# Optimization experiments

Measured on AMD Instinct MI355X. Metric: run time of the kernel, lower is better.

## Reference

```python
import jax, jax.numpy as jnp
import numpy as np

EMBED_DIM = 384
NUM_HEADS = 6
HEAD_DIM = EMBED_DIM // NUM_HEADS
MLP_HIDDEN = 4 * EMBED_DIM
LN_EPS = 1e-5


def layer_norm(x, gamma, beta):
    mu = jnp.mean(x, axis=-1, keepdims=True)
    var = jnp.mean((x - mu) ** 2, axis=-1, keepdims=True)
    return (x - mu) * jax.lax.rsqrt(var + LN_EPS) * gamma + beta


def setup_inputs() -> dict:
    key = jax.random.key(0)
    ks = jax.random.split(key, 8)
    D, H = EMBED_DIM, MLP_HIDDEN
    s = 1.0 / np.sqrt(D)
    sh = 1.0 / np.sqrt(H)
    return {
        "x": jax.random.normal(ks[0], (16, 1024, D), dtype=jnp.float32),
        "ln1_g": jnp.ones((D,), jnp.float32),
        "ln1_b": jnp.zeros((D,), jnp.float32),
        "qkv_w": jax.random.uniform(ks[1], (3 * D, D), jnp.float32, -s, s),
        "qkv_b": jax.random.uniform(ks[2], (3 * D,), jnp.float32, -s, s),
        "proj_w": jax.random.uniform(ks[3], (D, D), jnp.float32, -s, s),
        "proj_b": jax.random.uniform(ks[4], (D,), jnp.float32, -s, s),
        "ln2_g": jnp.ones((D,), jnp.float32),
        "ln2_b": jnp.zeros((D,), jnp.float32),
        "fc1_w": jax.random.uniform(ks[5], (H, D), jnp.float32, -s, s),
        "fc1_b": jax.random.uniform(ks[6], (H,), jnp.float32, -s, s),
        "fc2_w": jax.random.uniform(ks[7], (D, H), jnp.float32, -sh, sh),
        "fc2_b": jnp.zeros((D,), jnp.float32),
    }


def reference(x, ln1_g, ln1_b, qkv_w, qkv_b, proj_w, proj_b,
              ln2_g, ln2_b, fc1_w, fc1_b, fc2_w, fc2_b):
    B, N, D = x.shape
    Hh, Dh = NUM_HEADS, HEAD_DIM
    scale = Dh ** -0.5

    # --- attention sublayer (pre-norm) ---
    h = layer_norm(x, ln1_g, ln1_b)
    qkv = h @ qkv_w.T + qkv_b                      # [B,N,3D]
    qkv = qkv.reshape(B, N, 3, Hh, Dh)
    q, k, v = (qkv[:, :, i].transpose(0, 2, 1, 3) for i in range(3))  # [B,H,N,Dh]
    attn = jax.nn.softmax(jnp.einsum('bhnd,bhmd->bhnm', q, k) * scale, axis=-1)
    o = jnp.einsum('bhnm,bhmd->bhnd', attn, v)     # [B,H,N,Dh]
    o = o.transpose(0, 2, 1, 3).reshape(B, N, D)
    x = x + (o @ proj_w.T + proj_b)

    # --- MLP sublayer (pre-norm) ---
    h = layer_norm(x, ln2_g, ln2_b)
    h = jax.nn.gelu(h @ fc1_w.T + fc1_b, approximate=False)
    x = x + (h @ fc2_w.T + fc2_b)
    return x
```

## Files before the change

kernel.cpp:

```cpp
#include <hip/hip_runtime.h>

typedef unsigned short u16;
typedef unsigned int   u32;
typedef __bf16  bf16x8 __attribute__((ext_vector_type(8)));
typedef __bf16  bf16x4_t __attribute__((ext_vector_type(4)));
typedef float   f32x4  __attribute__((ext_vector_type(4)));
typedef float   f32x2  __attribute__((ext_vector_type(2)));

struct Ptrs { const void* p[13]; };

extern "C" __device__ float __ocml_native_exp2_f32(float);

__device__ __forceinline__ float bf2f(u16 u) {
    union { unsigned int i; float f; } c; c.i = ((unsigned int)u) << 16; return c.f;
}
__device__ __forceinline__ u16 f2bf(float f) {
    union { float f; unsigned int i; } c; c.f = f;
    unsigned int u = c.i;
    unsigned int r = (u + 0x7fffu + ((u >> 16) & 1u)) >> 16;
    return (u16)r;
}

__device__ __forceinline__ float wave_sum(float x) {
#pragma unroll
    for (int m = 32; m >= 1; m >>= 1) x += __shfl_xor(x, m);
    return x;
}

__device__ __forceinline__ void g2l16(const u16* g, u16* l) {
    __builtin_amdgcn_global_load_lds(
        (__attribute__((address_space(1))) void*)g,
        (__attribute__((address_space(3))) void*)l, 16, 0, 0);
}

__device__ __forceinline__ int sniff_bf16(const u32* __restrict__ w) {
    int cnt = 0;
    for (int i = 0; i < 32; ++i) {
        u16 lo = (u16)(w[i] & 0xFFFFu);
        int e = (lo >> 7) & 0xFF;
        cnt += (e >= 117 && e <= 123) ? 1 : 0;
    }
    return (cnt >= 16) ? 1 : 0;
}

__global__ __launch_bounds__(256) void k_cvt_ln1(Ptrs ps,
                                                 u16* __restrict__ cw,
                                                 int* __restrict__ flagp,
                                                 u16* __restrict__ cx,
                                                 u16* __restrict__ h)
{
    const int flag = sniff_bf16((const u32*)ps.p[3]);
    if (blockIdx.x == 0 && threadIdx.x == 0) *flagp = flag;

    if (blockIdx.x < 867) {
        const int cum[13] = {0,48,96,55392,55536,73968,74016,74064,74112,
                             147840,148032,221760,221808};
        const int off[12] = {0,384,768,443136,444288,591744,
                             592128,592512,592896,1182720,1184256,1774080};
        int c = blockIdx.x * 256 + threadIdx.x;
        if (c >= 221808) return;
        int seg = 0;
#pragma unroll
        for (int i = 1; i < 12; ++i) seg += (c >= cum[i]) ? 1 : 0;
        int e = (c - cum[seg]) * 8;
        u16* dst = cw + off[seg] + e;
        if (flag) {
            *(uint4*)dst = *((const uint4*)ps.p[seg + 1] + (e >> 3));
        } else {
            const float* s = (const float*)ps.p[seg + 1] + e;
            u16 tmp[8];
#pragma unroll
            for (int t = 0; t < 8; ++t) tmp[t] = f2bf(s[t]);
            *(uint4*)dst = *(const uint4*)tmp;
        }
        return;
    }

    const int wid = threadIdx.x >> 6, lane = threadIdx.x & 63;
    const int row = (blockIdx.x - 867) * 4 + wid;
    const int e0 = lane * 6;
    float v[6]; u16 raw[6];
    float gv[6], bv[6];
    if (flag) {
        const u16* p = (const u16*)ps.p[0] + (size_t)row * 384 + e0;
        u32 w0 = *(const u32*)(p);
        u32 w1 = *(const u32*)(p + 2);
        u32 w2 = *(const u32*)(p + 4);
        raw[0] = (u16)w0; raw[1] = (u16)(w0 >> 16);
        raw[2] = (u16)w1; raw[3] = (u16)(w1 >> 16);
        raw[4] = (u16)w2; raw[5] = (u16)(w2 >> 16);
#pragma unroll
        for (int t = 0; t < 6; t++) v[t] = bf2f(raw[t]);
        const u16* gp = (const u16*)ps.p[1] + e0;
        const u16* bp = (const u16*)ps.p[2] + e0;
#pragma unroll
        for (int t = 0; t < 6; t++) { gv[t] = bf2f(gp[t]); bv[t] = bf2f(bp[t]); }
    } else {
        const float* p = (const float*)ps.p[0] + (size_t)row * 384 + e0;
        f32x2 a0 = *(const f32x2*)(p);
        f32x2 a1 = *(const f32x2*)(p + 2);
        f32x2 a2 = *(const f32x2*)(p + 4);
        v[0] = a0[0]; v[1] = a0[1]; v[2] = a1[0];
        v[3] = a1[1]; v[4] = a2[0]; v[5] = a2[1];
#pragma unroll
        for (int t = 0; t < 6; t++) raw[t] = f2bf(v[t]);
        const float* gp = (const float*)ps.p[1] + e0;
        const float* bp = (const float*)ps.p[2] + e0;
#pragma unroll
        for (int t = 0; t < 6; t++) { gv[t] = gp[t]; bv[t] = bp[t]; }
    }
    u32* pc = (u32*)(cx + (size_t)row * 384 + e0);
    pc[0] = (u32)raw[0] | ((u32)raw[1] << 16);
    pc[1] = (u32)raw[2] | ((u32)raw[3] << 16);
    pc[2] = (u32)raw[4] | ((u32)raw[5] << 16);
    float s = 0.f;
#pragma unroll
    for (int t = 0; t < 6; t++) s += v[t];
    const float mu = wave_sum(s) * (1.0f / 384.0f);
    float vs = 0.f;
#pragma unroll
    for (int t = 0; t < 6; t++) { float d = v[t] - mu; vs += d * d; }
    const float var = wave_sum(vs) * (1.0f / 384.0f);
    const float rs = rsqrtf(var + 1e-5f);
    u16 ow[6];
#pragma unroll
    for (int t = 0; t < 6; t++)
        ow[t] = f2bf((v[t] - mu) * rs * gv[t] + bv[t]);
    u32* po = (u32*)(h + (size_t)row * 384 + e0);
    po[0] = (u32)ow[0] | ((u32)ow[1] << 16);
    po[1] = (u32)ow[2] | ((u32)ow[3] << 16);
    po[2] = (u32)ow[4] | ((u32)ow[5] << 16);
}

template <bool SWAP = false>
__device__ __forceinline__ void gemm_core_128_w8(const u16* __restrict__ A,
                                                 const u16* __restrict__ B,
                                                 int K, int m0, int n0,
                                                 f32x4 (&acc)[4][2])
{
    __shared__ __align__(16) u16 As[128 * 64];
    __shared__ __align__(16) u16 Bs[128 * 64];

    const int tid  = threadIdx.x;
    const int lane = tid & 63;
    const int wid  = tid >> 6;
    const int wm  = (wid >> 2) * 64;
    const int wn  = (wid & 3) * 32;
    const int l15 = lane & 15;
    const int g   = lane >> 4;
    const int srow   = lane >> 3;
    const int schunk = ((lane & 7) ^ srow) * 8;

    const u16* Abase = A + (size_t)(m0 + wid * 16 + srow) * K + schunk;
    const u16* Bbase = B + (size_t)(n0 + wid * 16 + srow) * K + schunk;

    for (int kk = 0; kk < K; kk += 64) {
        __syncthreads();
#pragma unroll
        for (int t = 0; t < 2; ++t) {
            g2l16(Abase + (size_t)t * 8 * K + kk, &As[(wid * 16 + t * 8) * 64]);
            g2l16(Bbase + (size_t)t * 8 * K + kk, &Bs[(wid * 16 + t * 8) * 64]);
        }
        __syncthreads();

#pragma unroll
        for (int ks = 0; ks < 2; ++ks) {
            const int p = ((ks * 4 + g) ^ (l15 & 7)) * 8;
            bf16x8 af[4], bfr[2];
#pragma unroll
            for (int i = 0; i < 4; i++)
                af[i] = __builtin_bit_cast(bf16x8,
                         *(const uint4*)&As[(wm + 16 * i + l15) * 64 + p]);
#pragma unroll
            for (int j = 0; j < 2; j++)
                bfr[j] = __builtin_bit_cast(bf16x8,
                         *(const uint4*)&Bs[(wn + 16 * j + l15) * 64 + p]);
#pragma unroll
            for (int i = 0; i < 4; i++)
#pragma unroll
                for (int j = 0; j < 2; j++) {
                    if (SWAP)
                        acc[i][j] = __builtin_amdgcn_mfma_f32_16x16x32_bf16(
                                        bfr[j], af[i], acc[i][j], 0, 0, 0);
                    else
                        acc[i][j] = __builtin_amdgcn_mfma_f32_16x16x32_bf16(
                                        af[i], bfr[j], acc[i][j], 0, 0, 0);
                }
        }
    }
}

__device__ __forceinline__ void gemm_core_128x64_w8(const u16* __restrict__ A,
                                                    const u16* __restrict__ B,
                                                    int K, int m0, int n0,
                                                    f32x4 (&acc)[2][2])
{
    __shared__ __align__(16) u16 As[128 * 64];
    __shared__ __align__(16) u16 Bs[64 * 64];

    const int tid  = threadIdx.x;
    const int lane = tid & 63;
    const int wid  = tid >> 6;
    const int wm  = (wid >> 1) * 32;
    const int wn  = (wid & 1) * 32;
    const int l15 = lane & 15;
    const int g   = lane >> 4;
    const int srow   = lane >> 3;
    const int schunk = ((lane & 7) ^ srow) * 8;

    const u16* Abase = A + (size_t)(m0 + wid * 16 + srow) * K + schunk;
    const u16* Bbase = B + (size_t)(n0 + wid * 8 + srow) * K + schunk;

    for (int kk = 0; kk < K; kk += 64) {
        __syncthreads();
#pragma unroll
        for (int t = 0; t < 2; ++t)
            g2l16(Abase + (size_t)t * 8 * K + kk, &As[(wid * 16 + t * 8) * 64]);
        g2l16(Bbase + kk, &Bs[(wid * 8) * 64]);
        __syncthreads();

#pragma unroll
        for (int ks = 0; ks < 2; ++ks) {
            const int p = ((ks * 4 + g) ^ (l15 & 7)) * 8;
            bf16x8 af[2], bfr[2];
#pragma unroll
            for (int i = 0; i < 2; i++)
                af[i] = __builtin_bit_cast(bf16x8,
                         *(const uint4*)&As[(wm + 16 * i + l15) * 64 + p]);
#pragma unroll
            for (int j = 0; j < 2; j++)
                bfr[j] = __builtin_bit_cast(bf16x8,
                         *(const uint4*)&Bs[(wn + 16 * j + l15) * 64 + p]);
#pragma unroll
            for (int i = 0; i < 2; i++)
#pragma unroll
                for (int j = 0; j < 2; j++)
                    acc[i][j] = __builtin_amdgcn_mfma_f32_16x16x32_bf16(
                                    af[i], bfr[j], acc[i][j], 0, 0, 0);
        }
    }
}

__global__ __launch_bounds__(256) void k_layernorm(const u16* __restrict__ in,
                                                   const u16* __restrict__ g,
                                                   const u16* __restrict__ b,
                                                   u16* __restrict__ out,
                                                   int nrows)
{
    const int wid = threadIdx.x >> 6, lane = threadIdx.x & 63;
    const int row = blockIdx.x * 4 + wid;
    if (row >= nrows) return;
    const int e0 = lane * 6;
    float v[6];
    const u16* p = in + (size_t)row * 384 + e0;
    u32 w0 = *(const u32*)(p);
    u32 w1 = *(const u32*)(p + 2);
    u32 w2 = *(const u32*)(p + 4);
    v[0] = bf2f((u16)w0); v[1] = bf2f((u16)(w0 >> 16));
    v[2] = bf2f((u16)w1); v[3] = bf2f((u16)(w1 >> 16));
    v[4] = bf2f((u16)w2); v[5] = bf2f((u16)(w2 >> 16));
    float s = 0.f;
#pragma unroll
    for (int t = 0; t < 6; t++) s += v[t];
    const float mu = wave_sum(s) * (1.0f / 384.0f);
    float vs = 0.f;
#pragma unroll
    for (int t = 0; t < 6; t++) { float d = v[t] - mu; vs += d * d; }
    const float var = wave_sum(vs) * (1.0f / 384.0f);
    const float rs = rsqrtf(var + 1e-5f);
    const u32* gg = (const u32*)(g + e0);
    const u32* bb = (const u32*)(b + e0);
    u32 gw[3] = {gg[0], gg[1], gg[2]};
    u32 bw[3] = {bb[0], bb[1], bb[2]};
    u16 ow[6];
#pragma unroll
    for (int t = 0; t < 6; t++) {
        u16 ge = (u16)(gw[t >> 1] >> ((t & 1) * 16));
        u16 be = (u16)(bw[t >> 1] >> ((t & 1) * 16));
        ow[t] = f2bf((v[t] - mu) * rs * bf2f(ge) + bf2f(be));
    }
    u32* po = (u32*)(out + (size_t)row * 384 + e0);
    po[0] = (u32)ow[0] | ((u32)ow[1] << 16);
    po[1] = (u32)ow[2] | ((u32)ow[3] << 16);
    po[2] = (u32)ow[4] | ((u32)ow[5] << 16);
}

__global__ __launch_bounds__(512) void k_gemm_qkv(const u16* __restrict__ A,
                                                  const u16* __restrict__ W,
                                                  const u16* __restrict__ bias,
                                                  u16* __restrict__ q,
                                                  u16* __restrict__ kbuf,
                                                  u16* __restrict__ vT)
{
    const int id = blockIdx.x, slot = id & 7, idx = id >> 3;
    const int m0 = (slot * 16 + idx / 9) * 128;
    const int n0 = (idx % 9) * 128;
    f32x4 acc[4][2];
#pragma unroll
    for (int i = 0; i < 4; i++)
#pragma unroll
        for (int j = 0; j < 2; j++) acc[i][j] = f32x4{0.f, 0.f, 0.f, 0.f};
    gemm_core_128_w8<true>(A, W, 384, m0, n0, acc);
    const int lane = threadIdx.x & 63, wid = threadIdx.x >> 6;
    const int wm = (wid >> 2) * 64, wn = (wid & 3) * 32;
    const int l15 = lane & 15, rq = (lane >> 4) * 4;
#pragma unroll
    for (int i = 0; i < 4; i++) {
        const int gr = m0 + wm + 16 * i + l15;
        const int bb = gr >> 10, nn = gr & 1023;
#pragma unroll
        for (int j = 0; j < 2; j++) {
            const int gcb = n0 + wn + 16 * j + rq;
            const int part = gcb / 384, rem = gcb % 384;
            const int head = rem >> 6, dhb = rem & 63;
            const int bh = bb * 6 + head;
            float vals[4];
#pragma unroll
            for (int r = 0; r < 4; r++) vals[r] = acc[i][j][r] + bf2f(bias[gcb + r]);
            if (part == 2) {
#pragma unroll
                for (int r = 0; r < 4; r++)
                    vT[((size_t)bh * 64 + dhb + r) * 1024 + nn] = f2bf(vals[r]);
            } else {
                u16* dst = part ? kbuf : q;
                u32 lo = (u32)f2bf(vals[0]) | ((u32)f2bf(vals[1]) << 16);
                u32 hi = (u32)f2bf(vals[2]) | ((u32)f2bf(vals[3]) << 16);
                uint2 pk; pk.x = lo; pk.y = hi;
                *(uint2*)&dst[((size_t)bh * 1024 + nn) * 64 + dhb] = pk;
            }
        }
    }
}

__global__ __launch_bounds__(512) void k_attn(const u16* __restrict__ q,
                                              const u16* __restrict__ kk,
                                              const u16* __restrict__ vT,
                                              u16* __restrict__ o)
{
    __shared__ __align__(16) u16 Ks[128 * 64];
    __shared__ __align__(16) u16 Vs[2][64 * 64];
    __shared__ __align__(16) u16 Ps[128 * 64];

    const int tid = threadIdx.x, lane = tid & 63, wid = tid >> 6;
    const int l15 = lane & 15, g = lane >> 4, q8 = g * 8;
    const int id = blockIdx.x;
    const int bh = (id & 7) * 12 + ((id >> 3) >> 3);
    const int q0 = ((id >> 3) & 7) * 128;
    const int wrow = wid * 16;

    const u16* Q = q  + (size_t)bh * 65536;
    const u16* K = kk + (size_t)bh * 65536;
    const u16* V = vT + (size_t)bh * 65536;

    const int srow   = lane >> 3;
    const int schunk = ((lane & 7) ^ srow) * 8;
    const int rd0 = ((0 + g) ^ (l15 & 7)) * 8;
    const int rd1 = ((4 + g) ^ (l15 & 7)) * 8;
    int pcol[4];
#pragma unroll
    for (int ip = 0; ip < 4; ++ip)
        pcol[ip] = (((ip * 2 + (g >> 1)) ^ (l15 & 7)) * 8) + (g & 1) * 4;

    bf16x8 aq[2];
#pragma unroll
    for (int ks = 0; ks < 2; ++ks) {
        bf16x8 t = __builtin_bit_cast(bf16x8,
            *(const uint4*)&Q[(size_t)(q0 + wrow + l15) * 64 + ks * 32 + q8]);
#pragma unroll
        for (int e = 0; e < 8; ++e)
            t[e] = (__bf16)((float)t[e] * 0.18033688f);
        aq[ks] = t;
    }

    f32x4 ob[4];
#pragma unroll
    for (int j = 0; j < 4; ++j) ob[j] = f32x4{0.f, 0.f, 0.f, 0.f};
    float lsum = 0.f;

    for (int kt2 = 0; kt2 < 8; ++kt2) {
        __syncthreads();
#pragma unroll
        for (int t = 0; t < 2; ++t) {
            int r0 = wid * 16 + t * 8;
            g2l16(&K[(size_t)(kt2 * 128 + r0 + srow) * 64 + schunk], &Ks[r0 * 64]);
        }
#pragma unroll
        for (int h = 0; h < 2; ++h) {
            int r0 = wid * 8;
            g2l16(&V[(size_t)(r0 + srow) * 1024 + kt2 * 128 + h * 64 + schunk],
                  &Vs[h][r0 * 64]);
        }
        __syncthreads();

#pragma unroll 1
        for (int h = 0; h < 2; ++h) {
            f32x4 st[4];
#pragma unroll
            for (int ip = 0; ip < 4; ++ip) st[ip] = f32x4{0.f, 0.f, 0.f, 0.f};
            __builtin_amdgcn_s_setprio(1);
#pragma unroll
            for (int ip = 0; ip < 4; ++ip) {
                int rbase = (h * 64 + ip * 16 + l15) * 64;
                bf16x8 bk0 = __builtin_bit_cast(bf16x8,
                    *(const uint4*)&Ks[rbase + rd0]);
                bf16x8 bk1 = __builtin_bit_cast(bf16x8,
                    *(const uint4*)&Ks[rbase + rd1]);
                st[ip] = __builtin_amdgcn_mfma_f32_16x16x32_bf16(
                            bk0, aq[0], st[ip], 0, 0, 0);
                st[ip] = __builtin_amdgcn_mfma_f32_16x16x32_bf16(
                            bk1, aq[1], st[ip], 0, 0, 0);
            }
            __builtin_amdgcn_s_setprio(0);

            float ps = 0.f;
#pragma unroll
            for (int ip = 0; ip < 4; ++ip)
#pragma unroll
                for (int r = 0; r < 4; ++r) {
                    float p = __ocml_native_exp2_f32(st[ip][r]);
                    st[ip][r] = p;
                    ps += p;
                }
            lsum += ps;

#pragma unroll
            for (int ip = 0; ip < 4; ++ip) {
                bf16x4_t pk;
#pragma unroll
                for (int r = 0; r < 4; ++r) pk[r] = (__bf16)st[ip][r];
                *(bf16x4_t*)&Ps[(wrow + l15) * 64 + pcol[ip]] = pk;
            }

            __builtin_amdgcn_s_setprio(1);
#pragma unroll
            for (int ks = 0; ks < 2; ++ks) {
                const int rdo = ks ? rd1 : rd0;
                bf16x8 ap = __builtin_bit_cast(bf16x8,
                    *(const uint4*)&Ps[(wrow + l15) * 64 + rdo]);
#pragma unroll
                for (int jv = 0; jv < 4; ++jv) {
                    bf16x8 bv = __builtin_bit_cast(bf16x8,
                        *(const uint4*)&Vs[h][(jv * 16 + l15) * 64 + rdo]);
                    ob[jv] = __builtin_amdgcn_mfma_f32_16x16x32_bf16(
                                ap, bv, ob[jv], 0, 0, 0);
                }
            }
            __builtin_amdgcn_s_setprio(0);
        }
    }

    lsum += __shfl_xor(lsum, 16);
    lsum += __shfl_xor(lsum, 32);
    const int bb = bh / 6, hh = bh % 6;
#pragma unroll
    for (int r = 0; r < 4; ++r) {
        int src = (lane & 48) | (g * 4 + r);
        float linv = 1.0f / __shfl(lsum, src);
        int row = q0 + wrow + g * 4 + r;
#pragma unroll
        for (int jv = 0; jv < 4; ++jv) {
            int dh = jv * 16 + l15;
            o[((size_t)(bb * 1024 + row)) * 384 + hh * 64 + dh] =
                f2bf(ob[jv][r] * linv);
        }
    }
}

__global__ __launch_bounds__(512) void k_gemm_proj(const u16* __restrict__ A,
                                                   const u16* __restrict__ W,
                                                   const u16* __restrict__ bias,
                                                   const u16* __restrict__ xin,
                                                   u16* __restrict__ x1)
{
    const int id = blockIdx.x, slot = id & 7, idx = id >> 3;
    const int m0 = (slot * 16 + idx / 6) * 128;
    const int n0 = (idx % 6) * 64;
    f32x4 acc[2][2];
#pragma unroll
    for (int i = 0; i < 2; i++)
#pragma unroll
        for (int j = 0; j < 2; j++) acc[i][j] = f32x4{0.f, 0.f, 0.f, 0.f};
    gemm_core_128x64_w8(A, W, 384, m0, n0, acc);
    const int lane = threadIdx.x & 63, wid = threadIdx.x >> 6;
    const int wm = (wid >> 1) * 32, wn = (wid & 1) * 32;
    const int l15 = lane & 15, rq = (lane >> 4) * 4;
#pragma unroll
    for (int i = 0; i < 2; i++)
#pragma unroll
        for (int j = 0; j < 2; j++)
#pragma unroll
            for (int r = 0; r < 4; r++) {
                int gr = m0 + wm + 16 * i + rq + r;
                int gc = n0 + wn + 16 * j + l15;
                size_t ix = (size_t)gr * 384 + gc;
                x1[ix] = f2bf(acc[i][j][r] + bf2f(bias[gc]) + bf2f(xin[ix]));
            }
}

__global__ __launch_bounds__(512) void k_gemm_fc1(const u16* __restrict__ A,
                                                  const u16* __restrict__ W,
                                                  const u16* __restrict__ bias,
                                                  u16* __restrict__ hmid)
{
    const int id = blockIdx.x, slot = id & 7, idx = id >> 3;
    const int m0 = (slot * 16 + idx / 12) * 128;
    const int n0 = (idx % 12) * 128;
    f32x4 acc[4][2];
#pragma unroll
    for (int i = 0; i < 4; i++)
#pragma unroll
        for (int j = 0; j < 2; j++) acc[i][j] = f32x4{0.f, 0.f, 0.f, 0.f};
    gemm_core_128_w8(A, W, 384, m0, n0, acc);
    const int lane = threadIdx.x & 63, wid = threadIdx.x >> 6;
    const int wm = (wid >> 2) * 64, wn = (wid & 3) * 32;
    const int l15 = lane & 15, rq = (lane >> 4) * 4;
#pragma unroll
    for (int i = 0; i < 4; i++)
#pragma unroll
        for (int j = 0; j < 2; j++)
#pragma unroll
            for (int r = 0; r < 4; r++) {
                int gr = m0 + wm + 16 * i + rq + r;
                int gc = n0 + wn + 16 * j + l15;
                float v = acc[i][j][r] + bf2f(bias[gc]);
                float u2 = v * (2.3022084f + 0.1029433f * v * v);
                float ge = v * __builtin_amdgcn_rcpf(
                               1.0f + __ocml_native_exp2_f32(-u2));
                hmid[(size_t)gr * 1536 + gc] = f2bf(ge);
            }
}

__global__ __launch_bounds__(512) void k_gemm_fc2(const u16* __restrict__ A,
                                                  const u16* __restrict__ W,
                                                  const u16* __restrict__ bias,
                                                  const u16* __restrict__ x1,
                                                  void* __restrict__ outv,
                                                  const int* __restrict__ flagp)
{
    const int id = blockIdx.x, slot = id & 7, idx = id >> 3;
    const int m0 = (slot * 16 + idx / 6) * 128;
    const int n0 = (idx % 6) * 64;
    f32x4 acc[2][2];
#pragma unroll
    for (int i = 0; i < 2; i++)
#pragma unroll
        for (int j = 0; j < 2; j++) acc[i][j] = f32x4{0.f, 0.f, 0.f, 0.f};
    gemm_core_128x64_w8(A, W, 1536, m0, n0, acc);
    const int lane = threadIdx.x & 63, wid = threadIdx.x >> 6;
    const int wm = (wid >> 1) * 32, wn = (wid & 1) * 32;
    const int l15 = lane & 15, rq = (lane >> 4) * 4;
    const int isbf = *flagp;
    u16*   ob = (u16*)outv;
    float* of = (float*)outv;
#pragma unroll
    for (int i = 0; i < 2; i++)
#pragma unroll
        for (int j = 0; j < 2; j++)
#pragma unroll
            for (int r = 0; r < 4; r++) {
                int gr = m0 + wm + 16 * i + rq + r;
                int gc = n0 + wn + 16 * j + l15;
                size_t ix = (size_t)gr * 384 + gc;
                float v = acc[i][j][r] + bf2f(bias[gc]) + bf2f(x1[ix]);
                if (isbf) ob[ix] = f2bf(v);
                else      of[ix] = v;
            }
}

extern "C" void kernel_launch(void* const* d_in, const int* in_sizes, int n_in,
                              void* d_out, int out_size, void* d_ws, size_t ws_size,
                              hipStream_t stream)
{
    char* ws = (char*)d_ws;
    u16*   cw   = (u16*)(ws + 0);
    int*   flag = (int*)(ws + 3548928);
    u16*   cx   = (u16*)(ws + 3549184);
    u16*   h    = (u16*)(ws + 16132096);
    u16*   x1   = (u16*)(ws + 28715008);
    u16*   q    = (u16*)(ws + 53880832);
    u16*   kbuf = (u16*)(ws + 66463744);
    u16*   vT   = (u16*)(ws + 79046656);
    u16*   o    = (u16*)(ws + 91629568);
    u16*   hmid = (u16*)(ws + 53880832);

    const u16* c_qkv_w  = cw + 768;
    const u16* c_qkv_b  = cw + 443136;
    const u16* c_proj_w = cw + 444288;
    const u16* c_proj_b = cw + 591744;
    const u16* c_ln2_g  = cw + 592128;
    const u16* c_ln2_b  = cw + 592512;
    const u16* c_fc1_w  = cw + 592896;
    const u16* c_fc1_b  = cw + 1182720;
    const u16* c_fc2_w  = cw + 1184256;
    const u16* c_fc2_b  = cw + 1774080;

    Ptrs ps;
    for (int i = 0; i < 13; ++i) ps.p[i] = d_in[i];

    k_cvt_ln1<<<4963, 256, 0, stream>>>(ps, cw, flag, cx, h);
    k_gemm_qkv<<<1152, 512, 0, stream>>>(h, c_qkv_w, c_qkv_b, q, kbuf, vT);
    k_attn<<<768, 512, 0, stream>>>(q, kbuf, vT, o);
    k_gemm_proj<<<768, 512, 0, stream>>>(o, c_proj_w, c_proj_b, cx, x1);
    k_layernorm<<<4096, 256, 0, stream>>>(x1, c_ln2_g, c_ln2_b, h, 16384);
    k_gemm_fc1<<<1536, 512, 0, stream>>>(h, c_fc1_w, c_fc1_b, hmid);
    k_gemm_fc2<<<768, 512, 0, stream>>>(hmid, c_fc2_w, c_fc2_b, x1,
                                        d_out, flag);
    (void)in_sizes; (void)n_in; (void)out_size; (void)ws_size; (void)c_fc2_b;
}
```

Baseline: 232.1 us.

## Double-buffer K/V tiles in attention kernel to overlap loads with MFMA compute

Splits the attention kernel's shared K and V buffers into two 64-key ping-pong buffers. The next tile is issued with async global-to-LDS copies while the current tile's QK, exp and PV MFMAs run. Each iteration now needs one barrier per 64-key tile instead of two barriers per 128-key block, so load latency is hidden behind compute. The cost is more barriers per key element and correctness that depends on the g2l16 copy having completed by the next barrier.

```diff
diff --git a/kernel.cpp b/kernel.cpp
--- a/kernel.cpp
+++ b/kernel.cpp
@@ -337,8 +337,10 @@
                                               const u16* __restrict__ vT,
                                               u16* __restrict__ o)
 {
-    __shared__ __align__(16) u16 Ks[128 * 64];
-    __shared__ __align__(16) u16 Vs[2][64 * 64];
+    __shared__ __align__(16) u16 Ks0[64 * 64];
+    __shared__ __align__(16) u16 Ks1[64 * 64];
+    __shared__ __align__(16) u16 Vs0[64 * 64];
+    __shared__ __align__(16) u16 Vs1[64 * 64];
     __shared__ __align__(16) u16 Ps[128 * 64];
 
     const int tid = threadIdx.x, lane = tid & 63, wid = tid >> 6;
@@ -361,6 +363,13 @@
     for (int ip = 0; ip < 4; ++ip)
         pcol[ip] = (((ip * 2 + (g >> 1)) ^ (l15 & 7)) * 8) + (g & 1) * 4;
 
+    const u16* Ksrc = K + (size_t)(wid * 8 + srow) * 64 + schunk;
+    const u16* Vsrc = V + (size_t)(wid * 8 + srow) * 1024 + schunk;
+    u16* Kd0 = &Ks0[(wid * 8) * 64];
+    u16* Kd1 = &Ks1[(wid * 8) * 64];
+    u16* Vd0 = &Vs0[(wid * 8) * 64];
+    u16* Vd1 = &Vs1[(wid * 8) * 64];
+
     bf16x8 aq[2];
 #pragma unroll
     for (int ks = 0; ks < 2; ++ks) {
@@ -377,76 +386,82 @@
     for (int j = 0; j < 4; ++j) ob[j] = f32x4{0.f, 0.f, 0.f, 0.f};
     float lsum = 0.f;
 
-    for (int kt2 = 0; kt2 < 8; ++kt2) {
+    auto compute = [&](const u16* Kbuf, const u16* Vbuf) {
+        f32x4 st[4];
+#pragma unroll
+        for (int ip = 0; ip < 4; ++ip) st[ip] = f32x4{0.f, 0.f, 0.f, 0.f};
+        __builtin_amdgcn_s_setprio(1);
+#pragma unroll
+        for (int ip = 0; ip < 4; ++ip) {
+            int rbase = (ip * 16 + l15) * 64;
+            bf16x8 bk0 = __builtin_bit_cast(bf16x8,
+                *(const uint4*)&Kbuf[rbase + rd0]);
+            bf16x8 bk1 = __builtin_bit_cast(bf16x8,
+                *(const uint4*)&Kbuf[rbase + rd1]);
+            st[ip] = __builtin_amdgcn_mfma_f32_16x16x32_bf16(
+                        bk0, aq[0], st[ip], 0, 0, 0);
+            st[ip] = __builtin_amdgcn_mfma_f32_16x16x32_bf16(
+                        bk1, aq[1], st[ip], 0, 0, 0);
+        }
+        __builtin_amdgcn_s_setprio(0);
+
+        float ps = 0.f;
+#pragma unroll
+        for (int ip = 0; ip < 4; ++ip)
+#pragma unroll
+            for (int r = 0; r < 4; ++r) {
+                float p = __ocml_native_exp2_f32(st[ip][r]);
+                st[ip][r] = p;
+                ps += p;
+            }
+        lsum += ps;
+
+#pragma unroll
+        for (int ip = 0; ip < 4; ++ip) {
+            bf16x4_t pk;
+#pragma unroll
+            for (int r = 0; r < 4; ++r) pk[r] = (__bf16)st[ip][r];
+            *(bf16x4_t*)&Ps[(wrow + l15) * 64 + pcol[ip]] = pk;
+        }
+
+        __builtin_amdgcn_s_setprio(1);
+#pragma unroll
+        for (int ks = 0; ks < 2; ++ks) {
+            const int rdo = ks ? rd1 : rd0;
+            bf16x8 ap = __builtin_bit_cast(bf16x8,
+                *(const uint4*)&Ps[(wrow + l15) * 64 + rdo]);
+#pragma unroll
+            for (int jv = 0; jv < 4; ++jv) {
+                bf16x8 bv = __builtin_bit_cast(bf16x8,
+                    *(const uint4*)&Vbuf[(jv * 16 + l15) * 64 + rdo]);
+                ob[jv] = __builtin_amdgcn_mfma_f32_16x16x32_bf16(
+                            ap, bv, ob[jv], 0, 0, 0);
+            }
+        }
+        __builtin_amdgcn_s_setprio(0);
+    };
+
+    g2l16(Ksrc, Kd0);
+    g2l16(Vsrc, Vd0);
+    __syncthreads();
+
+#pragma unroll 1
+    for (int k2 = 0; k2 < 8; ++k2) {
+        {
+            int nt = 2 * k2 + 1;
+            g2l16(Ksrc + (size_t)nt * 4096, Kd1);
+            g2l16(Vsrc + (size_t)nt * 64, Vd1);
+        }
+        compute(Ks0, Vs0);
         __syncthreads();
-#pragma unroll
-        for (int t = 0; t < 2; ++t) {
-            int r0 = wid * 16 + t * 8;
-            g2l16(&K[(size_t)(kt2 * 128 + r0 + srow) * 64 + schunk], &Ks[r0 * 64]);
-        }
-#pragma unroll
-        for (int h = 0; h < 2; ++h) {
-            int r0 = wid * 8;
-            g2l16(&V[(size_t)(r0 + srow) * 1024 + kt2 * 128 + h * 64 + schunk],
-                  &Vs[h][r0 * 64]);
-        }
+
+        if (k2 < 7) {
+            int nt = 2 * k2 + 2;
+            g2l16(Ksrc + (size_t)nt * 4096, Kd0);
+            g2l16(Vsrc + (size_t)nt * 64, Vd0);
+        }
+        compute(Ks1, Vs1);
         __syncthreads();
-
-#pragma unroll 1
-        for (int h = 0; h < 2; ++h) {
-            f32x4 st[4];
-#pragma unroll
-            for (int ip = 0; ip < 4; ++ip) st[ip] = f32x4{0.f, 0.f, 0.f, 0.f};
-            __builtin_amdgcn_s_setprio(1);
-#pragma unroll
-            for (int ip = 0; ip < 4; ++ip) {
-                int rbase = (h * 64 + ip * 16 + l15) * 64;
-                bf16x8 bk0 = __builtin_bit_cast(bf16x8,
-                    *(const uint4*)&Ks[rbase + rd0]);
-                bf16x8 bk1 = __builtin_bit_cast(bf16x8,
-                    *(const uint4*)&Ks[rbase + rd1]);
-                st[ip] = __builtin_amdgcn_mfma_f32_16x16x32_bf16(
-                            bk0, aq[0], st[ip], 0, 0, 0);
-                st[ip] = __builtin_amdgcn_mfma_f32_16x16x32_bf16(
-                            bk1, aq[1], st[ip], 0, 0, 0);
-            }
-            __builtin_amdgcn_s_setprio(0);
-
-            float ps = 0.f;
-#pragma unroll
-            for (int ip = 0; ip < 4; ++ip)
-#pragma unroll
-                for (int r = 0; r < 4; ++r) {
-                    float p = __ocml_native_exp2_f32(st[ip][r]);
-                    st[ip][r] = p;
-                    ps += p;
-                }
-            lsum += ps;
-
-#pragma unroll
-            for (int ip = 0; ip < 4; ++ip) {
-                bf16x4_t pk;
-#pragma unroll
-                for (int r = 0; r < 4; ++r) pk[r] = (__bf16)st[ip][r];
-                *(bf16x4_t*)&Ps[(wrow + l15) * 64 + pcol[ip]] = pk;
-            }
-
-            __builtin_amdgcn_s_setprio(1);
-#pragma unroll
-            for (int ks = 0; ks < 2; ++ks) {
-                const int rdo = ks ? rd1 : rd0;
-                bf16x8 ap = __builtin_bit_cast(bf16x8,
-                    *(const uint4*)&Ps[(wrow + l15) * 64 + rdo]);
-#pragma unroll
-                for (int jv = 0; jv < 4; ++jv) {
-                    bf16x8 bv = __builtin_bit_cast(bf16x8,
-                        *(const uint4*)&Vs[h][(jv * 16 + l15) * 64 + rdo]);
-                    ob[jv] = __builtin_amdgcn_mfma_f32_16x16x32_bf16(
-                                ap, bv, ob[jv], 0, 0, 0);
-                }
-            }
-            __builtin_amdgcn_s_setprio(0);
-        }
     }
 
     lsum += __shfl_xor(lsum, 16);
```

Result: slower. 242.4 us (+4.5%).
